# Kernel tuning notes

Hardware: AMD Instinct MI355X
Metric: run time of the kernel (lower is better)

The kernel has to match this reference:

```python
import jax, jax.numpy as jnp
import numpy as np

L, H, DK = 4, 8, 64
NEG = -1e9
PAD = -9999.0


def _ln(z, g, b, eps=1e-6):
    # LayerNormalization: uses unbiased std (torch default) and divides by (std + eps)
    m = jnp.mean(z, axis=-1, keepdims=True)
    s = jnp.std(z, axis=-1, keepdims=True, ddof=1)
    return g * (z - m) / (s + eps) + b


def _mha(q_in, kv_in, w, bw, pw, pb, lnp, mask):
    B, Sq, D = q_in.shape
    q = (q_in @ w[0] + bw[0]).reshape(B, Sq, H, DK).transpose(0, 2, 1, 3)
    k = (kv_in @ w[1] + bw[1]).reshape(B, -1, H, DK).transpose(0, 2, 1, 3)
    v = (kv_in @ w[2] + bw[2]).reshape(B, -1, H, DK).transpose(0, 2, 1, 3)
    scores = jnp.einsum('bhqd,bhkd->bhqk', q, k) * (1.0 / np.sqrt(DK))
    if mask is not None:
        scores = jnp.where(mask[:, None, :, :], NEG, scores)
    attn = jax.nn.softmax(scores, axis=-1)
    ctx = jnp.einsum('bhqk,bhkd->bhqd', attn, v).transpose(0, 2, 1, 3).reshape(B, Sq, H * DK)
    return _ln(q_in + ctx @ pw + pb, lnp[0], lnp[1])


def _ffn(x, w1, b1, w2, b2, lnp):
    # kernel-1 conv1d == pointwise linear; w1:[d_ff,d_model], w2:[d_model,d_ff]
    h = jax.nn.relu(jnp.einsum('bsd,fd->bsf', x, w1) + b1)
    o = jnp.einsum('bsf,df->bsd', h, w2) + b2
    return _ln(x + o, lnp[0], lnp[1])


def _forward(enc_inputs, dec_inputs, emb_w, emb_b, pos_table,
             e_qkv_w, e_qkv_b, e_pw, e_pb, e_ln1, e_w1, e_b1, e_w2, e_b2, e_ln2,
             ds_qkv_w, ds_qkv_b, ds_pw, ds_pb, d_ln1,
             dc_qkv_w, dc_qkv_b, dc_pw, dc_pb, d_ln2,
             d_w1, d_b1, d_w2, d_b2, d_ln3):
    B, Se, F = enc_inputs.shape
    Sd = dec_inputs.shape[1]
    # ConvEmbeddingLayer: kernel-1 conv producing (d_model - n_features) channels, concat with raw inputs
    enc = jnp.concatenate([enc_inputs, jnp.einsum('bsf,of->bso', enc_inputs, emb_w) + emb_b], axis=-1)
    dec = jnp.concatenate([dec_inputs, jnp.einsum('bsf,of->bso', dec_inputs, emb_w) + emb_b], axis=-1)
    # PosEncoding with full lengths -> rows 1..S of the padded table
    enc = enc + pos_table[1:Se + 1]
    dec = dec + pos_table[1:Sd + 1]
    # masks per get_attn_pad_mask / get_attn_subsequent_mask
    enc_pad = jnp.sum(enc_inputs, axis=-1) <= PAD  # [B,Se]
    dec_pad = jnp.sum(dec_inputs, axis=-1) <= PAD  # [B,Sd]
    enc_mask = jnp.broadcast_to(enc_pad[:, None, :], (B, Se, Se))
    causal = jnp.triu(jnp.ones((Sd, Sd), dtype=bool), 1)
    dec_self_mask = jnp.broadcast_to(dec_pad[:, None, :], (B, Sd, Sd)) | causal
    cross_mask = jnp.broadcast_to(enc_pad[:, None, :], (B, Sd, Se))
    for i in range(L):
        enc = _mha(enc, enc, e_qkv_w[i], e_qkv_b[i], e_pw[i], e_pb[i], e_ln1[i], enc_mask)
        enc = _ffn(enc, e_w1[i], e_b1[i], e_w2[i], e_b2[i], e_ln2[i])
    for i in range(L):
        dec = _mha(dec, dec, ds_qkv_w[i], ds_qkv_b[i], ds_pw[i], ds_pb[i], d_ln1[i], dec_self_mask)
        dec = _mha(dec, enc, dc_qkv_w[i], dc_qkv_b[i], dc_pw[i], dc_pb[i], d_ln2[i], cross_mask)
        dec = _ffn(dec, d_w1[i], d_b1[i], d_w2[i], d_b2[i], d_ln3[i])
    return dec


def setup_inputs() -> dict:
    B, Se, Sd, F, Dm, Dff = 8, 512, 512, 32, 512, 2048
    key = jax.random.key(0)
    ks = iter(jax.random.split(key, 32))
    s = 0.02

    def n(shape, sc=s):
        return jax.random.normal(next(ks), shape, jnp.float32) * sc

    # sinusoidal PosEncoding table with leading pad row
    pos = np.arange(Se, dtype=np.float64)[:, None]
    j = np.arange(Dm)[None, :]
    ang = pos / np.power(10000.0, 2.0 * (j // 2) / Dm)
    ang[:, 0::2] = np.sin(ang[:, 0::2])
    ang[:, 1::2] = np.cos(ang[:, 1::2])
    pos_table = jnp.asarray(np.concatenate([np.zeros((1, Dm)), ang]).astype(np.float32))

    ln = jnp.broadcast_to(jnp.stack([jnp.ones(Dm), jnp.zeros(Dm)]), (L, 2, Dm)).astype(jnp.float32) + 0.0
    return {
        'enc_inputs': jax.random.normal(next(ks), (B, Se, F), jnp.float32),
        'dec_inputs': jax.random.normal(next(ks), (B, Sd, F), jnp.float32),
        'emb_w': n((Dm - F, F)), 'emb_b': jnp.zeros(Dm - F, jnp.float32),
        'pos_table': pos_table,
        'e_qkv_w': n((L, 3, Dm, H * DK)), 'e_qkv_b': jnp.zeros((L, 3, H * DK), jnp.float32),
        'e_pw': n((L, H * DK, Dm)), 'e_pb': jnp.zeros((L, Dm), jnp.float32), 'e_ln1': ln,
        'e_w1': n((L, Dff, Dm)), 'e_b1': jnp.zeros((L, Dff), jnp.float32),
        'e_w2': n((L, Dm, Dff)), 'e_b2': jnp.zeros((L, Dm), jnp.float32), 'e_ln2': ln,
        'ds_qkv_w': n((L, 3, Dm, H * DK)), 'ds_qkv_b': jnp.zeros((L, 3, H * DK), jnp.float32),
        'ds_pw': n((L, H * DK, Dm)), 'ds_pb': jnp.zeros((L, Dm), jnp.float32), 'd_ln1': ln,
        'dc_qkv_w': n((L, 3, Dm, H * DK)), 'dc_qkv_b': jnp.zeros((L, 3, H * DK), jnp.float32),
        'dc_pw': n((L, H * DK, Dm)), 'dc_pb': jnp.zeros((L, Dm), jnp.float32), 'd_ln2': ln,
        'd_w1': n((L, Dff, Dm)), 'd_b1': jnp.zeros((L, Dff), jnp.float32),
        'd_w2': n((L, Dm, Dff)), 'd_b2': jnp.zeros((L, Dm), jnp.float32), 'd_ln3': ln,
    }


def reference(enc_inputs, dec_inputs, emb_w, emb_b, pos_table,
              e_qkv_w, e_qkv_b, e_pw, e_pb, e_ln1, e_w1, e_b1, e_w2, e_b2, e_ln2,
              ds_qkv_w, ds_qkv_b, ds_pw, ds_pb, d_ln1,
              dc_qkv_w, dc_qkv_b, dc_pw, dc_pb, d_ln2,
              d_w1, d_b1, d_w2, d_b2, d_ln3):
    return _forward(enc_inputs, dec_inputs, emb_w, emb_b, pos_table,
                    e_qkv_w, e_qkv_b, e_pw, e_pb, e_ln1, e_w1, e_b1, e_w2, e_b2, e_ln2,
                    ds_qkv_w, ds_qkv_b, ds_pw, ds_pb, d_ln1,
                    dc_qkv_w, dc_qkv_b, dc_pw, dc_pb, d_ln2,
                    d_w1, d_b1, d_w2, d_b2, d_ln3)
```

## Files before the change

### kernel.cpp

```cpp
#include <hip/hip_runtime.h>
#include <cstdint>
#include <cstddef>

typedef unsigned short u16;
typedef __bf16 bf16x8 __attribute__((ext_vector_type(8)));
typedef float f32x4 __attribute__((ext_vector_type(4)));

constexpr int Bz = 8, Sq = 512, Hh = 8, DKd = 64, Dm = 512, Dff = 2048, NL = 4;
constexpr int TOK = Bz * Sq;
constexpr size_t MAT = (size_t)512 * 512;
constexpr size_t EL  = (size_t)TOK * Dm;
constexpr size_t WFT = (size_t)Dff * Dm;

__device__ __forceinline__ float bf2f(u16 u) {
  union { uint32_t i; float f; } v; v.i = (uint32_t)u << 16; return v.f;
}
__device__ __forceinline__ u16 f2bf(float f) {
  union { float f; uint32_t i; } v; v.f = f;
  uint32_t i = v.i;
  i += 0x7fffu + ((i >> 16) & 1u);
  return (u16)(i >> 16);
}

__device__ __forceinline__ void gload16(const u16* g, u16* l) {
  __builtin_amdgcn_global_load_lds(
      (const __attribute__((address_space(1))) unsigned int*)g,
      (__attribute__((address_space(3))) unsigned int*)l, 16, 0, 0);
}

template<int BM, int BN>
__global__ __launch_bounds__(256)
void gemm_tile(const u16* __restrict__ A, const u16* __restrict__ Bt,
               const float* __restrict__ bias, u16* __restrict__ C,
               int K, int lda, long long sA, int ldb, long long sB,
               int ldc, long long sC, int cmode, int relu, int colofs,
               const u16* A2, int xsplit, const float* __restrict__ posp)
{
  constexpr int HM = BM / 2, HN = BN / 2, MI = HM / 16, NI = HN / 16;
  __shared__ __align__(16) u16 As[BM * 64];
  __shared__ __align__(16) u16 Bs[BN * 64];
  const int bz = blockIdx.z;
  const u16* Abase = A;
  int colbase;
  if (A2 && (int)blockIdx.x >= xsplit) {
    Abase = A2;
    colbase = 512 + ((int)blockIdx.x - xsplit) * BN;
  } else {
    colbase = colofs + (int)blockIdx.x * BN;
  }
  const u16* Ab = Abase + (size_t)bz * (size_t)sA + (size_t)(blockIdx.y * BM) * lda;
  const u16* Bb = Bt + (size_t)bz * (size_t)sB + (size_t)colbase * ldb;
  const int tid  = threadIdx.x;
  const int lane = tid & 63;
  const int wid  = tid >> 6;
  const int l15  = lane & 15;
  const int quad = lane >> 4;
  const int wm   = wid >> 1, wn = wid & 1;

  f32x4 acc[MI][NI] = {};

  for (int k0 = 0; k0 < K; k0 += 64) {
#pragma unroll
    for (int i = 0; i < BM / 32; ++i) {
      const int s = tid + i * 256;
      const int row = s >> 3, c = (s & 7) ^ (row & 7);
      gload16(Ab + (size_t)row * lda + k0 + c * 8, As + s * 8);
    }
#pragma unroll
    for (int i = 0; i < BN / 32; ++i) {
      const int s = tid + i * 256;
      const int row = s >> 3, c = (s & 7) ^ (row & 7);
      gload16(Bb + (size_t)row * ldb + k0 + c * 8, Bs + s * 8);
    }
    __syncthreads();
#pragma unroll
    for (int kk = 0; kk < 2; ++kk) {
      bf16x8 af[MI], bfr[NI];
#pragma unroll
      for (int mi = 0; mi < MI; ++mi) {
        const int ra = wm * HM + mi * 16 + l15;
        af[mi] = *(const bf16x8*)(As + ra * 64 + (((kk * 4 + quad) ^ (ra & 7))) * 8);
      }
#pragma unroll
      for (int ni = 0; ni < NI; ++ni) {
        const int rb = wn * HN + ni * 16 + l15;
        bfr[ni] = *(const bf16x8*)(Bs + rb * 64 + (((kk * 4 + quad) ^ (rb & 7))) * 8);
      }
#pragma unroll
      for (int mi = 0; mi < MI; ++mi)
#pragma unroll
        for (int ni = 0; ni < NI; ++ni)
          acc[mi][ni] = __builtin_amdgcn_mfma_f32_16x16x32_bf16(af[mi], bfr[ni], acc[mi][ni], 0, 0, 0);
    }
    __syncthreads();
  }

  const int rblk = blockIdx.y * BM + wm * HM + quad * 4;
#pragma unroll
  for (int ni = 0; ni < NI; ++ni) {
    const int colx = colbase + wn * HN + ni * 16 + l15;
    const float bv = bias ? bias[colx] : 0.f;
#pragma unroll
    for (int mi = 0; mi < MI; ++mi) {
#pragma unroll
      for (int r = 0; r < 4; ++r) {
        float v = acc[mi][ni][r] + bv;
        if (relu) v = fmaxf(v, 0.f);
        const int grow = rblk + mi * 16 + r;
        size_t off;
        if (cmode == 0) {
          off = (size_t)bz * (size_t)sC + (size_t)grow * ldc + colx;
        } else if (cmode == 5) {
          const int s = grow & 511;
          v += posp[(size_t)(s + 1) * 512 + colx];
          off = (size_t)grow * 512 + colx;
        } else {
          const int sec = colx >> 9, n = colx & 511, h = n >> 6, d = n & 63;
          const int b = grow >> 9, s = grow & 511;
          if (sec == 0) v *= 0.125f;
          if (sec < 2) off = (size_t)sec * EL + (size_t)b * 262144 + (size_t)h * 32768 + (size_t)s * 64 + d;
          else         off = 2 * EL + (size_t)b * 262144 + (size_t)h * 32768 + (size_t)d * 512 + s;
        }
        C[off] = f2bf(v);
      }
    }
  }
}

__global__ __launch_bounds__(256)
void flash_attn(const u16* __restrict__ q, const u16* __restrict__ k,
                const u16* __restrict__ v, const unsigned char* __restrict__ pad,
                u16* __restrict__ ctx, int mtype)
{
  __shared__ __align__(16) u16 KVs[8192];
  __shared__ __align__(16) u16 Pw[4][2048];
  const int bh = blockIdx.y, b = bh >> 3, h = bh & 7;
  const int qt = blockIdx.x;
  const int tid = threadIdx.x, lane = tid & 63, wid = tid >> 6;
  const int l15 = lane & 15, quad = lane >> 4;
  const size_t bho = (size_t)bh * 32768;
  const int qrow = qt * 64 + wid * 16 + l15;
  const int qcd  = qt * 64 + wid * 16 + quad * 4;

  unsigned char* Ps = (unsigned char*)&Pw[0][0];
  if (tid < 128) ((uchar4*)Ps)[tid] = ((const uchar4*)(pad + b * 512))[tid];

  bf16x8 aq0 = *(const bf16x8*)(q + bho + (size_t)qrow * 64 + quad * 8);
  bf16x8 aq1 = *(const bf16x8*)(q + bho + (size_t)qrow * 64 + 32 + quad * 8);

  f32x4 S[32];
#pragma unroll
  for (int kc = 0; kc < 4; ++kc) {
    __syncthreads();
#pragma unroll
    for (int i = 0; i < 4; ++i) {
      const int s = tid + i * 256;
      const int row = s >> 3, c = (s & 7) ^ (row & 7);
      gload16(k + bho + (size_t)(kc * 128 + row) * 64 + c * 8, KVs + s * 8);
    }
    __syncthreads();
#pragma unroll
    for (int t = 0; t < 8; ++t) {
      const int sw = l15 & 7;
      bf16x8 b0 = *(const bf16x8*)(KVs + (t * 16 + l15) * 64 + (quad ^ sw) * 8);
      bf16x8 b1 = *(const bf16x8*)(KVs + (t * 16 + l15) * 64 + ((4 + quad) ^ sw) * 8);
      f32x4 z = {0.f, 0.f, 0.f, 0.f};
      z = __builtin_amdgcn_mfma_f32_16x16x32_bf16(aq0, b0, z, 0, 0, 0);
      S[kc * 8 + t] = __builtin_amdgcn_mfma_f32_16x16x32_bf16(aq1, b1, z, 0, 0, 0);
    }
  }

  unsigned pm = 0u;
#pragma unroll
  for (int t = 0; t < 32; ++t) pm |= (unsigned)(Ps[t * 16 + l15] != 0) << t;

  float inv[4];
#pragma unroll
  for (int r = 0; r < 4; ++r) {
    const int qg = qcd + r;
    float mx = -3.0e38f;
#pragma unroll
    for (int t = 0; t < 32; ++t) {
      const int col = t * 16 + l15;
      const bool m = ((pm >> t) & 1u) || (mtype == 1 && col > qg);
      const float val = m ? -1e9f : S[t][r];
      S[t][r] = val;
      mx = fmaxf(mx, val);
    }
#pragma unroll
    for (int o = 8; o > 0; o >>= 1) mx = fmaxf(mx, __shfl_xor(mx, o));
    float sm = 0.f;
#pragma unroll
    for (int t = 0; t < 32; ++t) { const float e = __expf(S[t][r] - mx); S[t][r] = e; sm += e; }
#pragma unroll
    for (int o = 8; o > 0; o >>= 1) sm += __shfl_xor(sm, o);
    inv[r] = 1.f / sm;
  }

  f32x4 O[4] = {};
  u16* myP = &Pw[wid][0];
#pragma unroll
  for (int kc = 0; kc < 4; ++kc) {
    __syncthreads();
#pragma unroll
    for (int i = 0; i < 4; ++i) {
      const int s = tid + i * 256;
      const int row = s >> 4, c = (s & 15) ^ (row & 15);
      gload16(v + bho + (size_t)row * 512 + kc * 128 + c * 8, KVs + s * 8);
    }
#pragma unroll
    for (int t = 0; t < 8; ++t)
#pragma unroll
      for (int r = 0; r < 4; ++r) {
        const int rowq = quad * 4 + r;
        const int c = 2 * t + (l15 >> 3);
        myP[rowq * 128 + (c ^ rowq) * 8 + (l15 & 7)] = f2bf(S[kc * 8 + t][r] * inv[r]);
      }
    __syncthreads();
#pragma unroll
    for (int kk = 0; kk < 4; ++kk) {
      bf16x8 ap = *(const bf16x8*)(myP + l15 * 128 + ((kk * 4 + quad) ^ l15) * 8);
#pragma unroll
      for (int ni = 0; ni < 4; ++ni) {
        bf16x8 bv = *(const bf16x8*)(KVs + (ni * 16 + l15) * 128 + ((kk * 4 + quad) ^ l15) * 8);
        O[ni] = __builtin_amdgcn_mfma_f32_16x16x32_bf16(ap, bv, O[ni], 0, 0, 0);
      }
    }
  }

  const int token = b * 512 + qcd;
#pragma unroll
  for (int ni = 0; ni < 4; ++ni)
#pragma unroll
    for (int r = 0; r < 4; ++r)
      ctx[(size_t)(token + r) * 512 + h * 64 + ni * 16 + l15] = f2bf(O[ni][r]);
}

__global__ __launch_bounds__(256)
void prep_weights(const float* __restrict__ s0, const float* __restrict__ s1,
                  const float* __restrict__ s2, const float* __restrict__ s3,
                  const float* __restrict__ s4, const float* __restrict__ s5,
                  u16* __restrict__ outT,
                  const float* __restrict__ c0, const float* __restrict__ c1,
                  const float* __restrict__ c2, const float* __restrict__ c3,
                  u16* __restrict__ outC,
                  const float* __restrict__ ew, const float* __restrict__ eb,
                  u16* __restrict__ ewb, float* __restrict__ biasE,
                  const float* __restrict__ xe, const float* __restrict__ xd,
                  u16* __restrict__ xbf,
                  unsigned char* __restrict__ pe, unsigned char* __restrict__ pd)
{
  __shared__ float tile[32][33];
  const int z = blockIdx.z;
  const int tid = threadIdx.y * 32 + threadIdx.x;
  if (z < 48) {
    const float* src; int zi;
    if      (z < 12) { src = s0; zi = z; }
    else if (z < 24) { src = s1; zi = z - 12; }
    else if (z < 36) { src = s2; zi = z - 24; }
    else if (z < 40) { src = s3; zi = z - 36; }
    else if (z < 44) { src = s4; zi = z - 40; }
    else             { src = s5; zi = z - 44; }
    const float* in = src + (size_t)zi * MAT;
    u16* o = outT + (size_t)z * MAT;
    const int x = blockIdx.x * 32 + threadIdx.x;
    const int y = blockIdx.y * 32 + threadIdx.y;
#pragma unroll
    for (int i = 0; i < 32; i += 8)
      tile[threadIdx.y + i][threadIdx.x] = in[(size_t)(y + i) * 512 + x];
    __syncthreads();
    const int r  = tid >> 3;
    const int cg = (tid & 7) * 4;
    ushort4 w;
    w.x = f2bf(tile[cg + 0][r]);
    w.y = f2bf(tile[cg + 1][r]);
    w.z = f2bf(tile[cg + 2][r]);
    w.w = f2bf(tile[cg + 3][r]);
    *(ushort4*)(o + (size_t)(blockIdx.x * 32 + r) * 512 + blockIdx.y * 32 + cg) = w;
  } else if (z < 112) {
    const int L = (z - 48) * 256 + blockIdx.y * 16 + blockIdx.x;
    const int tens = L >> 12, bx = L & 4095;
    const float* srcs[4] = { c0, c1, c2, c3 };
    const float* src = srcs[tens];
    u16* dst = outC + (size_t)tens * (4 * WFT);
    const int i = (bx * 256 + tid) * 4;
    float4 v = *(const float4*)(src + i);
    ushort4 u = { f2bf(v.x), f2bf(v.y), f2bf(v.z), f2bf(v.w) };
    *(ushort4*)(dst + i) = u;
  } else if (z == 112) {
    const int bxy = blockIdx.y * 16 + blockIdx.x;
    if (tid < 128) {
      const int row = bxy * 2 + (tid >> 6);
      const int c = tid & 63;
      float v;
      if (row < 32) v = (c == row) ? 1.f : 0.f;
      else          v = (c < 32) ? ew[(size_t)(row - 32) * 32 + c] : 0.f;
      ewb[(size_t)row * 64 + c] = f2bf(v);
    }
    if (bxy == 0) {
#pragma unroll
      for (int rep = 0; rep < 2; ++rep) {
        const int i = tid + rep * 256;
        biasE[i] = (i < 32) ? 0.f : eb[i - 32];
      }
    }
  } else {
    const int bxy = blockIdx.y * 16 + blockIdx.x;
    const int lw = tid & 31;
#pragma unroll
    for (int rep = 0; rep < 4; ++rep) {
      const int r = bxy * 32 + rep * 8 + (tid >> 5);
      const float* xsrc = (r < 4096) ? xe : xd;
      const int rr = r & 4095;
      const float v = xsrc[(size_t)rr * 32 + lw];
      float sm = v;
#pragma unroll
      for (int o = 16; o > 0; o >>= 1) sm += __shfl_xor(sm, o);
      if (lw == 0) {
        unsigned char* pv = (r < 4096) ? pe : pd;
        pv[rr] = (sm <= -9999.f) ? 1 : 0;
      }
      u16* orow = xbf + (size_t)r * 64;
      orow[lw] = f2bf(v);
      orow[32 + lw] = 0;
    }
  }
}

__global__ __launch_bounds__(256)
void add_ln(const u16* __restrict__ x, const u16* __restrict__ y,
            const float* __restrict__ g, const float* __restrict__ bb,
            u16* __restrict__ out, float* __restrict__ out32)
{
  const int row  = blockIdx.x * 4 + (threadIdx.x >> 6);
  const int lane = threadIdx.x & 63;
  const int c0 = lane * 8;
  const size_t base = (size_t)row * Dm + c0;

  uint4 xr = *(const uint4*)(x + base);
  uint4 yr = *(const uint4*)(y + base);
  const u16* xh = (const u16*)&xr;
  const u16* yh = (const u16*)&yr;
  float z[8];
  float s = 0.f;
#pragma unroll
  for (int j = 0; j < 8; ++j) { z[j] = bf2f(xh[j]) + bf2f(yh[j]); s += z[j]; }
#pragma unroll
  for (int off = 32; off > 0; off >>= 1) s += __shfl_xor(s, off);
  const float mean = s * (1.f / 512.f);
  float ss = 0.f;
#pragma unroll
  for (int j = 0; j < 8; ++j) { z[j] -= mean; ss += z[j] * z[j]; }
#pragma unroll
  for (int off = 32; off > 0; off >>= 1) ss += __shfl_xor(ss, off);
  const float stdv = sqrtf(ss * (1.f / 511.f));
  const float inv = 1.f / (stdv + 1e-6f);

  float4 g0 = *(const float4*)(g + c0),  g1 = *(const float4*)(g + c0 + 4);
  float4 b0 = *(const float4*)(bb + c0), b1 = *(const float4*)(bb + c0 + 4);
  float gv[8] = { g0.x, g0.y, g0.z, g0.w, g1.x, g1.y, g1.z, g1.w };
  float bv[8] = { b0.x, b0.y, b0.z, b0.w, b1.x, b1.y, b1.z, b1.w };
  float o[8];
#pragma unroll
  for (int j = 0; j < 8; ++j) o[j] = gv[j] * z[j] * inv + bv[j];
  if (out32) {
    float4 w0 = { o[0], o[1], o[2], o[3] };
    float4 w1 = { o[4], o[5], o[6], o[7] };
    *(float4*)(out32 + base) = w0;
    *(float4*)(out32 + base + 4) = w1;
  } else {
    uint4 ow;
    u16* oh = (u16*)&ow;
#pragma unroll
    for (int j = 0; j < 8; ++j) oh[j] = f2bf(o[j]);
    *(uint4*)(out + base) = ow;
  }
}

extern "C" void kernel_launch(void* const* d_in, const int* in_sizes, int n_in,
                              void* d_out, int out_size, void* d_ws, size_t ws_size,
                              hipStream_t stream)
{
  (void)in_sizes; (void)n_in; (void)out_size;
  const float* enc_in   = (const float*)d_in[0];
  const float* dec_in   = (const float*)d_in[1];
  const float* emb_w    = (const float*)d_in[2];
  const float* emb_b    = (const float*)d_in[3];
  const float* pos      = (const float*)d_in[4];
  const float* e_qkv_w  = (const float*)d_in[5];
  const float* e_qkv_b  = (const float*)d_in[6];
  const float* e_pw     = (const float*)d_in[7];
  const float* e_pb     = (const float*)d_in[8];
  const float* e_ln1    = (const float*)d_in[9];
  const float* e_w1     = (const float*)d_in[10];
  const float* e_b1     = (const float*)d_in[11];
  const float* e_w2     = (const float*)d_in[12];
  const float* e_b2     = (const float*)d_in[13];
  const float* e_ln2    = (const float*)d_in[14];
  const float* ds_qkv_w = (const float*)d_in[15];
  const float* ds_qkv_b = (const float*)d_in[16];
  const float* ds_pw    = (const float*)d_in[17];
  const float* ds_pb    = (const float*)d_in[18];
  const float* d_ln1    = (const float*)d_in[19];
  const float* dc_qkv_w = (const float*)d_in[20];
  const float* dc_qkv_b = (const float*)d_in[21];
  const float* dc_pw    = (const float*)d_in[22];
  const float* dc_pb    = (const float*)d_in[23];
  const float* d_ln2    = (const float*)d_in[24];
  const float* d_w1     = (const float*)d_in[25];
  const float* d_b1     = (const float*)d_in[26];
  const float* d_w2     = (const float*)d_in[27];
  const float* d_b2     = (const float*)d_in[28];
  const float* d_ln3    = (const float*)d_in[29];

  u16* ws  = (u16*)d_ws;
  u16* enc = ws;
  u16* dec = ws + EL;
  u16* qb  = ws + 2 * EL;
  u16* kb  = ws + 3 * EL;
  u16* vT  = ws + 4 * EL;
  u16* ctx = ws + 5 * EL;
  u16* t1  = ws + 6 * EL;
  u16* hff = ws + 7 * EL;
  u16* wT  = ws + 15 * EL;
  unsigned char* padE = (unsigned char*)(ws + 21 * EL);
  unsigned char* padD = padE + TOK;
  u16* xbf   = ws + 21 * EL + 8192;
  u16* ewb   = xbf + (size_t)8192 * 64;
  float* biasE = (float*)(ewb + 32768);
  u16* wfAll = ws + 22 * EL;
  if (ws_size < 30 * EL * 2 + 2 * TOK) return;

  prep_weights<<<dim3(16, 16, 114), dim3(32, 8), 0, stream>>>(
      e_qkv_w, ds_qkv_w, dc_qkv_w, e_pw, ds_pw, dc_pw, wT,
      e_w1, e_w2, d_w1, d_w2, wfAll,
      emb_w, emb_b, ewb, biasE,
      enc_in, dec_in, xbf, padE, padD);
  gemm_tile<64, 128><<<dim3(4, 128, 1), 256, 0, stream>>>(
      xbf, ewb, biasE, enc, 64, 64, 0, 64, 0, 512, 0, 5, 0, 0, nullptr, 0, pos);

  auto attention = [&](const u16* qsrc, const u16* kvsrc, const u16* wq3, const float* b3,
                       const u16* pwT, const float* pb, const float* ln,
                       const unsigned char* pad, int mtype, u16* x) {
    if (qsrc == kvsrc) {
      gemm_tile<64, 128><<<dim3(12, 64, 1), 256, 0, stream>>>(
          qsrc, wq3, b3, qb, 512, 512, 0, 512, 0, 0, 0, 4, 0, 0, nullptr, 0, nullptr);
    } else {
      gemm_tile<64, 128><<<dim3(12, 64, 1), 256, 0, stream>>>(
          qsrc, wq3, b3, qb, 512, 512, 0, 512, 0, 0, 0, 4, 0, 0, kvsrc, 4, nullptr);
    }
    flash_attn<<<dim3(8, 64), 256, 0, stream>>>(qb, kb, vT, pad, ctx, mtype);
    gemm_tile<64, 64><<<dim3(8, 64, 1), 256, 0, stream>>>(
        ctx, pwT, pb, t1, 512, 512, 0, 512, 0, 512, 0, 0, 0, 0, nullptr, 0, nullptr);
    add_ln<<<TOK / 4, 256, 0, stream>>>(x, t1, ln, ln + 512, x, nullptr);
  };

  auto ffn = [&](u16* x, const u16* w1b, const float* b1, const u16* w2b,
                 const float* b2, const float* ln, float* o32) {
    gemm_tile<128, 128><<<dim3(16, 32, 1), 256, 0, stream>>>(
        x, w1b, b1, hff, 512, 512, 0, 512, 0, 2048, 0, 0, 1, 0, nullptr, 0, nullptr);
    gemm_tile<64, 64><<<dim3(8, 64, 1), 256, 0, stream>>>(
        hff, w2b, b2, t1, 2048, 2048, 0, 2048, 0, 512, 0, 0, 0, 0, nullptr, 0, nullptr);
    add_ln<<<TOK / 4, 256, 0, stream>>>(x, t1, ln, ln + 512, x, o32);
  };

  for (int i = 0; i < NL; ++i) {
    attention(enc, enc, wT + (size_t)(i * 3) * MAT, e_qkv_b + i * 3 * 512,
              wT + (size_t)(36 + i) * MAT, e_pb + i * 512, e_ln1 + i * 1024, padE, 0, enc);
    ffn(enc, wfAll + (size_t)i * WFT, e_b1 + i * Dff,
        wfAll + 4 * WFT + (size_t)i * WFT, e_b2 + i * Dm, e_ln2 + i * 1024, nullptr);
  }

  for (int i = 0; i < NL; ++i) {
    attention(dec, dec, wT + (size_t)(12 + i * 3) * MAT, ds_qkv_b + i * 3 * 512,
              wT + (size_t)(40 + i) * MAT, ds_pb + i * 512, d_ln1 + i * 1024, padD, 1, dec);
    attention(dec, enc, wT + (size_t)(24 + i * 3) * MAT, dc_qkv_b + i * 3 * 512,
              wT + (size_t)(44 + i) * MAT, dc_pb + i * 512, d_ln2 + i * 1024, padE, 2, dec);
    ffn(dec, wfAll + 8 * WFT + (size_t)i * WFT, d_b1 + i * Dff,
        wfAll + 12 * WFT + (size_t)i * WFT, d_b2 + i * Dm, d_ln3 + i * 1024,
        (i == NL - 1) ? (float*)d_out : nullptr);
  }
}
```

Baseline: 1.282 ms.

## Double-buffer GEMM LDS tiles to overlap global loads with MFMA compute

```diff
diff --git a/kernel.cpp b/kernel.cpp
--- a/kernel.cpp
+++ b/kernel.cpp
@@ -28,7 +28,7 @@
       (__attribute__((address_space(3))) unsigned int*)l, 16, 0, 0);
 }
 
-template<int BM, int BN>
+template<int BM, int BN, int TAG>
 __global__ __launch_bounds__(256)
 void gemm_tile(const u16* __restrict__ A, const u16* __restrict__ Bt,
                const float* __restrict__ bias, u16* __restrict__ C,
@@ -37,8 +37,10 @@
                const u16* A2, int xsplit, const float* __restrict__ posp)
 {
   constexpr int HM = BM / 2, HN = BN / 2, MI = HM / 16, NI = HN / 16;
-  __shared__ __align__(16) u16 As[BM * 64];
-  __shared__ __align__(16) u16 Bs[BN * 64];
+  constexpr int LV = BM / 32 + BN / 32;
+  static_assert(LV == 4 || LV == 6 || LV == 8, "unsupported tile");
+  __shared__ __align__(16) u16 As[2][BM * 64];
+  __shared__ __align__(16) u16 Bs[2][BN * 64];
   const int bz = blockIdx.z;
   const u16* Abase = A;
   int colbase;
@@ -52,39 +54,41 @@
   const u16* Bb = Bt + (size_t)bz * (size_t)sB + (size_t)colbase * ldb;
   const int tid  = threadIdx.x;
   const int lane = tid & 63;
-  const int wid  = tid >> 6;
   const int l15  = lane & 15;
   const int quad = lane >> 4;
+  const int wid  = tid >> 6;
   const int wm   = wid >> 1, wn = wid & 1;
 
   f32x4 acc[MI][NI] = {};
 
-  for (int k0 = 0; k0 < K; k0 += 64) {
+  auto STAGE = [&](int buf, int k0) {
 #pragma unroll
     for (int i = 0; i < BM / 32; ++i) {
       const int s = tid + i * 256;
       const int row = s >> 3, c = (s & 7) ^ (row & 7);
-      gload16(Ab + (size_t)row * lda + k0 + c * 8, As + s * 8);
+      gload16(Ab + (size_t)row * lda + k0 + c * 8, &As[buf][s * 8]);
     }
 #pragma unroll
     for (int i = 0; i < BN / 32; ++i) {
       const int s = tid + i * 256;
       const int row = s >> 3, c = (s & 7) ^ (row & 7);
-      gload16(Bb + (size_t)row * ldb + k0 + c * 8, Bs + s * 8);
-    }
-    __syncthreads();
+      gload16(Bb + (size_t)row * ldb + k0 + c * 8, &Bs[buf][s * 8]);
+    }
+  };
+
+  auto COMPUTE = [&](int buf) {
 #pragma unroll
     for (int kk = 0; kk < 2; ++kk) {
       bf16x8 af[MI], bfr[NI];
 #pragma unroll
       for (int mi = 0; mi < MI; ++mi) {
         const int ra = wm * HM + mi * 16 + l15;
-        af[mi] = *(const bf16x8*)(As + ra * 64 + (((kk * 4 + quad) ^ (ra & 7))) * 8);
+        af[mi] = *(const bf16x8*)(&As[buf][ra * 64 + (((kk * 4 + quad) ^ (ra & 7))) * 8]);
       }
 #pragma unroll
       for (int ni = 0; ni < NI; ++ni) {
         const int rb = wn * HN + ni * 16 + l15;
-        bfr[ni] = *(const bf16x8*)(Bs + rb * 64 + (((kk * 4 + quad) ^ (rb & 7))) * 8);
+        bfr[ni] = *(const bf16x8*)(&Bs[buf][rb * 64 + (((kk * 4 + quad) ^ (rb & 7))) * 8]);
       }
 #pragma unroll
       for (int mi = 0; mi < MI; ++mi)
@@ -92,8 +96,25 @@
         for (int ni = 0; ni < NI; ++ni)
           acc[mi][ni] = __builtin_amdgcn_mfma_f32_16x16x32_bf16(af[mi], bfr[ni], acc[mi][ni], 0, 0, 0);
     }
-    __syncthreads();
-  }
+  };
+
+  STAGE(0, 0);
+  const int NT = K >> 6;
+  int cur = 0;
+  for (int t = 0; t < NT - 1; ++t) {
+    STAGE(cur ^ 1, (t + 1) << 6);
+    if constexpr (LV == 4)      asm volatile("s_waitcnt vmcnt(4)" ::: "memory");
+    else if constexpr (LV == 6) asm volatile("s_waitcnt vmcnt(6)" ::: "memory");
+    else                        asm volatile("s_waitcnt vmcnt(8)" ::: "memory");
+    __builtin_amdgcn_s_barrier();
+    COMPUTE(cur);
+    asm volatile("s_waitcnt lgkmcnt(0)" ::: "memory");
+    __builtin_amdgcn_s_barrier();
+    cur ^= 1;
+  }
+  asm volatile("s_waitcnt vmcnt(0)" ::: "memory");
+  __builtin_amdgcn_s_barrier();
+  COMPUTE(cur);
 
   const int rblk = blockIdx.y * BM + wm * HM + quad * 4;
 #pragma unroll
@@ -253,6 +274,8 @@
   __shared__ float tile[32][33];
   const int z = blockIdx.z;
   const int tid = threadIdx.y * 32 + threadIdx.x;
+  const int r  = tid >> 3;
+  const int c4 = (tid & 7) * 4;
   if (z < 48) {
     const float* src; int zi;
     if      (z < 12) { src = s0; zi = z; }
@@ -263,20 +286,16 @@
     else             { src = s5; zi = z - 44; }
     const float* in = src + (size_t)zi * MAT;
     u16* o = outT + (size_t)z * MAT;
-    const int x = blockIdx.x * 32 + threadIdx.x;
-    const int y = blockIdx.y * 32 + threadIdx.y;
-#pragma unroll
-    for (int i = 0; i < 32; i += 8)
-      tile[threadIdx.y + i][threadIdx.x] = in[(size_t)(y + i) * 512 + x];
+    float4 v = *(const float4*)(in + (size_t)(blockIdx.y * 32 + r) * 512 + blockIdx.x * 32 + c4);
+    tile[r][c4 + 0] = v.x; tile[r][c4 + 1] = v.y;
+    tile[r][c4 + 2] = v.z; tile[r][c4 + 3] = v.w;
     __syncthreads();
-    const int r  = tid >> 3;
-    const int cg = (tid & 7) * 4;
     ushort4 w;
-    w.x = f2bf(tile[cg + 0][r]);
-    w.y = f2bf(tile[cg + 1][r]);
-    w.z = f2bf(tile[cg + 2][r]);
-    w.w = f2bf(tile[cg + 3][r]);
-    *(ushort4*)(o + (size_t)(blockIdx.x * 32 + r) * 512 + blockIdx.y * 32 + cg) = w;
+    w.x = f2bf(tile[c4 + 0][r]);
+    w.y = f2bf(tile[c4 + 1][r]);
+    w.z = f2bf(tile[c4 + 2][r]);
+    w.w = f2bf(tile[c4 + 3][r]);
+    *(ushort4*)(o + (size_t)(blockIdx.x * 32 + r) * 512 + blockIdx.y * 32 + c4) = w;
   } else if (z < 112) {
     const int L = (z - 48) * 256 + blockIdx.y * 16 + blockIdx.x;
     const int tens = L >> 12, bx = L & 4095;
@@ -309,18 +328,18 @@
     const int lw = tid & 31;
 #pragma unroll
     for (int rep = 0; rep < 4; ++rep) {
-      const int r = bxy * 32 + rep * 8 + (tid >> 5);
-      const float* xsrc = (r < 4096) ? xe : xd;
-      const int rr = r & 4095;
+      const int rr0 = bxy * 32 + rep * 8 + (tid >> 5);
+      const float* xsrc = (rr0 < 4096) ? xe : xd;
+      const int rr = rr0 & 4095;
       const float v = xsrc[(size_t)rr * 32 + lw];
       float sm = v;
 #pragma unroll
       for (int o = 16; o > 0; o >>= 1) sm += __shfl_xor(sm, o);
       if (lw == 0) {
-        unsigned char* pv = (r < 4096) ? pe : pd;
+        unsigned char* pv = (rr0 < 4096) ? pe : pd;
         pv[rr] = (sm <= -9999.f) ? 1 : 0;
       }
-      u16* orow = xbf + (size_t)r * 64;
+      u16* orow = xbf + (size_t)rr0 * 64;
       orow[lw] = f2bf(v);
       orow[32 + lw] = 0;
     }
@@ -436,30 +455,30 @@
       e_w1, e_w2, d_w1, d_w2, wfAll,
       emb_w, emb_b, ewb, biasE,
       enc_in, dec_in, xbf, padE, padD);
-  gemm_tile<64, 128><<<dim3(4, 128, 1), 256, 0, stream>>>(
+  gemm_tile<64, 128, 4><<<dim3(4, 128, 1), 256, 0, stream>>>(
       xbf, ewb, biasE, enc, 64, 64, 0, 64, 0, 512, 0, 5, 0, 0, nullptr, 0, pos);
 
   auto attention = [&](const u16* qsrc, const u16* kvsrc, const u16* wq3, const float* b3,
                        const u16* pwT, const float* pb, const float* ln,
                        const unsigned char* pad, int mtype, u16* x) {
     if (qsrc == kvsrc) {
-      gemm_tile<64, 128><<<dim3(12, 64, 1), 256, 0, stream>>>(
+      gemm_tile<64, 128, 0><<<dim3(12, 64, 1), 256, 0, stream>>>(
           qsrc, wq3, b3, qb, 512, 512, 0, 512, 0, 0, 0, 4, 0, 0, nullptr, 0, nullptr);
     } else {
-      gemm_tile<64, 128><<<dim3(12, 64, 1), 256, 0, stream>>>(
+      gemm_tile<64, 128, 0><<<dim3(12, 64, 1), 256, 0, stream>>>(
           qsrc, wq3, b3, qb, 512, 512, 0, 512, 0, 0, 0, 4, 0, 0, kvsrc, 4, nullptr);
     }
     flash_attn<<<dim3(8, 64), 256, 0, stream>>>(qb, kb, vT, pad, ctx, mtype);
-    gemm_tile<64, 64><<<dim3(8, 64, 1), 256, 0, stream>>>(
+    gemm_tile<64, 64, 1><<<dim3(8, 64, 1), 256, 0, stream>>>(
         ctx, pwT, pb, t1, 512, 512, 0, 512, 0, 512, 0, 0, 0, 0, nullptr, 0, nullptr);
     add_ln<<<TOK / 4, 256, 0, stream>>>(x, t1, ln, ln + 512, x, nullptr);
   };
 
   auto ffn = [&](u16* x, const u16* w1b, const float* b1, const u16* w2b,
                  const float* b2, const float* ln, float* o32) {
-    gemm_tile<128, 128><<<dim3(16, 32, 1), 256, 0, stream>>>(
+    gemm_tile<64, 128, 2><<<dim3(16, 64, 1), 256, 0, stream>>>(
         x, w1b, b1, hff, 512, 512, 0, 512, 0, 2048, 0, 0, 1, 0, nullptr, 0, nullptr);
-    gemm_tile<64, 64><<<dim3(8, 64, 1), 256, 0, stream>>>(
+    gemm_tile<64, 64, 3><<<dim3(8, 64, 1), 256, 0, stream>>>(
         hff, w2b, b2, t1, 2048, 2048, 0, 2048, 0, 512, 0, 0, 0, 0, nullptr, 0, nullptr);
     add_ln<<<TOK / 4, 256, 0, stream>>>(x, t1, ln, ln + 512, x, o32);
   };
```

New measurement: 1.294 ms. Within noise of the previous version (+0.9%).

## Fuse output-projection and FFN2 GEMMs with residual add and LayerNorm

Applied to the files above, without the earlier changes.

```diff
diff --git a/kernel.cpp b/kernel.cpp
--- a/kernel.cpp
+++ b/kernel.cpp
@@ -28,7 +28,7 @@
       (__attribute__((address_space(3))) unsigned int*)l, 16, 0, 0);
 }
 
-template<int BM, int BN>
+template<int BM, int BN, int TAG>
 __global__ __launch_bounds__(256)
 void gemm_tile(const u16* __restrict__ A, const u16* __restrict__ Bt,
                const float* __restrict__ bias, u16* __restrict__ C,
@@ -127,6 +127,124 @@
   }
 }
 
+template<int K, int TAG>
+__global__ __launch_bounds__(256)
+void gemm_row_ln(const u16* __restrict__ A, const u16* __restrict__ Bt,
+                 const float* __restrict__ bias, const u16* __restrict__ resid,
+                 const float* __restrict__ g, const float* __restrict__ bb,
+                 u16* __restrict__ out, float* __restrict__ out32)
+{
+  __shared__ __align__(16) u16 Bs[512 * 64];
+  __shared__ __align__(16) u16 As[16 * 64];
+  __shared__ float redS[4][16], redQ[4][16];
+  const int tid = threadIdx.x, lane = tid & 63, wid = tid >> 6;
+  const int l15 = lane & 15, quad = lane >> 4;
+  const int r0 = blockIdx.x * 16;
+  const u16* Ab = A + (size_t)r0 * K;
+
+  f32x4 acc[8] = {};
+  for (int k0 = 0; k0 < K; k0 += 64) {
+    if (tid < 128) {
+      const int row = tid >> 3, c = (tid & 7) ^ (row & 7);
+      gload16(Ab + (size_t)row * K + k0 + c * 8, As + tid * 8);
+    }
+#pragma unroll
+    for (int i = 0; i < 16; ++i) {
+      const int s = tid + i * 256;
+      const int row = s >> 3, c = (s & 7) ^ (row & 7);
+      gload16(Bt + (size_t)row * K + k0 + c * 8, Bs + s * 8);
+    }
+    __syncthreads();
+#pragma unroll
+    for (int kk = 0; kk < 2; ++kk) {
+      bf16x8 af = *(const bf16x8*)(As + l15 * 64 + (((kk * 4 + quad) ^ (l15 & 7))) * 8);
+#pragma unroll
+      for (int ni = 0; ni < 8; ++ni) {
+        const int rb = wid * 128 + ni * 16 + l15;
+        bf16x8 bf = *(const bf16x8*)(Bs + rb * 64 + (((kk * 4 + quad) ^ (rb & 7))) * 8);
+        acc[ni] = __builtin_amdgcn_mfma_f32_16x16x32_bf16(af, bf, acc[ni], 0, 0, 0);
+      }
+    }
+    __syncthreads();
+  }
+
+  float z[8][4];
+  float s[4] = {0.f, 0.f, 0.f, 0.f}, q[4] = {0.f, 0.f, 0.f, 0.f};
+#pragma unroll
+  for (int ni = 0; ni < 8; ++ni) {
+    const int colx = wid * 128 + ni * 16 + l15;
+    const float bv = bias[colx];
+#pragma unroll
+    for (int r = 0; r < 4; ++r) {
+      const int row = quad * 4 + r;
+      const float zz = acc[ni][r] + bv + bf2f(resid[(size_t)(r0 + row) * 512 + colx]);
+      z[ni][r] = zz; s[r] += zz; q[r] += zz * zz;
+    }
+  }
+#pragma unroll
+  for (int r = 0; r < 4; ++r) {
+#pragma unroll
+    for (int m = 8; m > 0; m >>= 1) {
+      s[r] += __shfl_xor(s[r], m);
+      q[r] += __shfl_xor(q[r], m);
+    }
+  }
+  if (l15 == 0) {
+#pragma unroll
+    for (int r = 0; r < 4; ++r) {
+      redS[wid][quad * 4 + r] = s[r];
+      redQ[wid][quad * 4 + r] = q[r];
+    }
+  }
+  __syncthreads();
+  float mean[4], inv[4];
+#pragma unroll
+  for (int r = 0; r < 4; ++r) {
+    const int row = quad * 4 + r;
+    const float sT = redS[0][row] + redS[1][row] + redS[2][row] + redS[3][row];
+    const float qT = redQ[0][row] + redQ[1][row] + redQ[2][row] + redQ[3][row];
+    mean[r] = sT * (1.f / 512.f);
+    const float ssc = fmaxf(qT - 512.f * mean[r] * mean[r], 0.f);
+    const float stdv = sqrtf(ssc * (1.f / 511.f));
+    inv[r] = 1.f / (stdv + 1e-6f);
+  }
+  __syncthreads();
+  u16* Ls = Bs;
+#pragma unroll
+  for (int ni = 0; ni < 8; ++ni) {
+    const int colx = wid * 128 + ni * 16 + l15;
+    const float gv = g[colx], bvv = bb[colx];
+#pragma unroll
+    for (int r = 0; r < 4; ++r) {
+      const int row = quad * 4 + r;
+      Ls[row * 512 + colx] = f2bf(gv * (z[ni][r] - mean[r]) * inv[r] + bvv);
+    }
+  }
+  __syncthreads();
+  if (out32) {
+#pragma unroll
+    for (int i = 0; i < 4; ++i) {
+      const int idx = tid + i * 256;
+      const int row = idx >> 6, c8 = idx & 63;
+      uint4 raw = *(const uint4*)(Ls + (size_t)row * 512 + c8 * 8);
+      const u16* h = (const u16*)&raw;
+      float4 o0 = { bf2f(h[0]), bf2f(h[1]), bf2f(h[2]), bf2f(h[3]) };
+      float4 o1 = { bf2f(h[4]), bf2f(h[5]), bf2f(h[6]), bf2f(h[7]) };
+      float* dst = out32 + (size_t)(r0 + row) * 512 + c8 * 8;
+      *(float4*)dst = o0;
+      *(float4*)(dst + 4) = o1;
+    }
+  } else {
+#pragma unroll
+    for (int i = 0; i < 4; ++i) {
+      const int idx = tid + i * 256;
+      const int row = idx >> 6, c8 = idx & 63;
+      *(uint4*)(out + (size_t)(r0 + row) * 512 + c8 * 8) =
+          *(const uint4*)(Ls + (size_t)row * 512 + c8 * 8);
+    }
+  }
+}
+
 __global__ __launch_bounds__(256)
 void flash_attn(const u16* __restrict__ q, const u16* __restrict__ k,
                 const u16* __restrict__ v, const unsigned char* __restrict__ pad,
@@ -250,10 +368,12 @@
                   u16* __restrict__ xbf,
                   unsigned char* __restrict__ pe, unsigned char* __restrict__ pd)
 {
-  __shared__ float tile[32][33];
-  const int z = blockIdx.z;
-  const int tid = threadIdx.y * 32 + threadIdx.x;
-  if (z < 48) {
+  __shared__ float tile[64][65];
+  const int blk = blockIdx.x;
+  const int tid = threadIdx.x;
+  if (blk < 3072) {
+    const int z = blk >> 6, t = blk & 63;
+    const int tx = t & 7, ty = t >> 3;
     const float* src; int zi;
     if      (z < 12) { src = s0; zi = z; }
     else if (z < 24) { src = s1; zi = z - 12; }
@@ -263,117 +383,75 @@
     else             { src = s5; zi = z - 44; }
     const float* in = src + (size_t)zi * MAT;
     u16* o = outT + (size_t)z * MAT;
-    const int x = blockIdx.x * 32 + threadIdx.x;
-    const int y = blockIdx.y * 32 + threadIdx.y;
-#pragma unroll
-    for (int i = 0; i < 32; i += 8)
-      tile[threadIdx.y + i][threadIdx.x] = in[(size_t)(y + i) * 512 + x];
-    __syncthreads();
-    const int r  = tid >> 3;
-    const int cg = (tid & 7) * 4;
-    ushort4 w;
-    w.x = f2bf(tile[cg + 0][r]);
-    w.y = f2bf(tile[cg + 1][r]);
-    w.z = f2bf(tile[cg + 2][r]);
-    w.w = f2bf(tile[cg + 3][r]);
-    *(ushort4*)(o + (size_t)(blockIdx.x * 32 + r) * 512 + blockIdx.y * 32 + cg) = w;
-  } else if (z < 112) {
-    const int L = (z - 48) * 256 + blockIdx.y * 16 + blockIdx.x;
-    const int tens = L >> 12, bx = L & 4095;
+    const int rr = tid >> 4, slot = tid & 15;
+#pragma unroll
+    for (int j = 0; j < 4; ++j) {
+      const int row = j * 16 + rr;
+      float4 v = *(const float4*)(in + (size_t)(ty * 64 + row) * 512 + tx * 64 + slot * 4);
+      tile[row][slot * 4 + 0] = v.x; tile[row][slot * 4 + 1] = v.y;
+      tile[row][slot * 4 + 2] = v.z; tile[row][slot * 4 + 3] = v.w;
+    }
+    __syncthreads();
+#pragma unroll
+    for (int j = 0; j < 4; ++j) {
+      const int row = j * 16 + rr;
+      ushort4 w;
+      w.x = f2bf(tile[slot * 4 + 0][row]);
+      w.y = f2bf(tile[slot * 4 + 1][row]);
+      w.z = f2bf(tile[slot * 4 + 2][row]);
+      w.w = f2bf(tile[slot * 4 + 3][row]);
+      *(ushort4*)(o + (size_t)(tx * 64 + row) * 512 + ty * 64 + slot * 4) = w;
+    }
+  } else if (blk < 7168) {
+    const int L = blk - 3072;
+    const size_t e0 = (size_t)L * 4096 + (size_t)tid * 16;
+    const int tens = (int)(e0 >> 22);
+    const size_t local = e0 & (4 * WFT - 1);
     const float* srcs[4] = { c0, c1, c2, c3 };
     const float* src = srcs[tens];
-    u16* dst = outC + (size_t)tens * (4 * WFT);
-    const int i = (bx * 256 + tid) * 4;
-    float4 v = *(const float4*)(src + i);
-    ushort4 u = { f2bf(v.x), f2bf(v.y), f2bf(v.z), f2bf(v.w) };
-    *(ushort4*)(dst + i) = u;
-  } else if (z == 112) {
-    const int bxy = blockIdx.y * 16 + blockIdx.x;
-    if (tid < 128) {
-      const int row = bxy * 2 + (tid >> 6);
-      const int c = tid & 63;
+    u16* dst = outC + (size_t)tens * (4 * WFT) + local;
+#pragma unroll
+    for (int j = 0; j < 4; ++j) {
+      float4 v = *(const float4*)(src + local + j * 4);
+      ushort4 u = { f2bf(v.x), f2bf(v.y), f2bf(v.z), f2bf(v.w) };
+      *(ushort4*)(dst + j * 4) = u;
+    }
+  } else if (blk < 7184) {
+    const int j = blk - 7168;
+    const int row = j * 32 + (tid >> 3);
+    const int c0i = (tid & 7) * 8;
+#pragma unroll
+    for (int k = 0; k < 8; ++k) {
+      const int c = c0i + k;
       float v;
       if (row < 32) v = (c == row) ? 1.f : 0.f;
       else          v = (c < 32) ? ew[(size_t)(row - 32) * 32 + c] : 0.f;
       ewb[(size_t)row * 64 + c] = f2bf(v);
     }
-    if (bxy == 0) {
-#pragma unroll
-      for (int rep = 0; rep < 2; ++rep) {
-        const int i = tid + rep * 256;
-        biasE[i] = (i < 32) ? 0.f : eb[i - 32];
-      }
+    if (j == 0) {
+      biasE[tid]       = (tid < 32) ? 0.f : eb[tid - 32];
+      biasE[tid + 256] = eb[tid + 256 - 32];
     }
   } else {
-    const int bxy = blockIdx.y * 16 + blockIdx.x;
+    const int bxy = blk - 7184;
     const int lw = tid & 31;
 #pragma unroll
     for (int rep = 0; rep < 4; ++rep) {
-      const int r = bxy * 32 + rep * 8 + (tid >> 5);
-      const float* xsrc = (r < 4096) ? xe : xd;
-      const int rr = r & 4095;
+      const int rr0 = bxy * 32 + rep * 8 + (tid >> 5);
+      const float* xsrc = (rr0 < 4096) ? xe : xd;
+      const int rr = rr0 & 4095;
       const float v = xsrc[(size_t)rr * 32 + lw];
       float sm = v;
 #pragma unroll
       for (int o = 16; o > 0; o >>= 1) sm += __shfl_xor(sm, o);
       if (lw == 0) {
-        unsigned char* pv = (r < 4096) ? pe : pd;
+        unsigned char* pv = (rr0 < 4096) ? pe : pd;
         pv[rr] = (sm <= -9999.f) ? 1 : 0;
       }
-      u16* orow = xbf + (size_t)r * 64;
+      u16* orow = xbf + (size_t)rr0 * 64;
       orow[lw] = f2bf(v);
       orow[32 + lw] = 0;
     }
-  }
-}
-
-__global__ __launch_bounds__(256)
-void add_ln(const u16* __restrict__ x, const u16* __restrict__ y,
-            const float* __restrict__ g, const float* __restrict__ bb,
-            u16* __restrict__ out, float* __restrict__ out32)
-{
-  const int row  = blockIdx.x * 4 + (threadIdx.x >> 6);
-  const int lane = threadIdx.x & 63;
-  const int c0 = lane * 8;
-  const size_t base = (size_t)row * Dm + c0;
-
-  uint4 xr = *(const uint4*)(x + base);
-  uint4 yr = *(const uint4*)(y + base);
-  const u16* xh = (const u16*)&xr;
-  const u16* yh = (const u16*)&yr;
-  float z[8];
-  float s = 0.f;
-#pragma unroll
-  for (int j = 0; j < 8; ++j) { z[j] = bf2f(xh[j]) + bf2f(yh[j]); s += z[j]; }
-#pragma unroll
-  for (int off = 32; off > 0; off >>= 1) s += __shfl_xor(s, off);
-  const float mean = s * (1.f / 512.f);
-  float ss = 0.f;
-#pragma unroll
-  for (int j = 0; j < 8; ++j) { z[j] -= mean; ss += z[j] * z[j]; }
-#pragma unroll
-  for (int off = 32; off > 0; off >>= 1) ss += __shfl_xor(ss, off);
-  const float stdv = sqrtf(ss * (1.f / 511.f));
-  const float inv = 1.f / (stdv + 1e-6f);
-
-  float4 g0 = *(const float4*)(g + c0),  g1 = *(const float4*)(g + c0 + 4);
-  float4 b0 = *(const float4*)(bb + c0), b1 = *(const float4*)(bb + c0 + 4);
-  float gv[8] = { g0.x, g0.y, g0.z, g0.w, g1.x, g1.y, g1.z, g1.w };
-  float bv[8] = { b0.x, b0.y, b0.z, b0.w, b1.x, b1.y, b1.z, b1.w };
-  float o[8];
-#pragma unroll
-  for (int j = 0; j < 8; ++j) o[j] = gv[j] * z[j] * inv + bv[j];
-  if (out32) {
-    float4 w0 = { o[0], o[1], o[2], o[3] };
-    float4 w1 = { o[4], o[5], o[6], o[7] };
-    *(float4*)(out32 + base) = w0;
-    *(float4*)(out32 + base + 4) = w1;
-  } else {
-    uint4 ow;
-    u16* oh = (u16*)&ow;
-#pragma unroll
-    for (int j = 0; j < 8; ++j) oh[j] = f2bf(o[j]);
-    *(uint4*)(out + base) = ow;
   }
 }
 
@@ -420,7 +498,6 @@
   u16* kb  = ws + 3 * EL;
   u16* vT  = ws + 4 * EL;
   u16* ctx = ws + 5 * EL;
-  u16* t1  = ws + 6 * EL;
   u16* hff = ws + 7 * EL;
   u16* wT  = ws + 15 * EL;
   unsigned char* padE = (unsigned char*)(ws + 21 * EL);
@@ -431,37 +508,35 @@
   u16* wfAll = ws + 22 * EL;
   if (ws_size < 30 * EL * 2 + 2 * TOK) return;
 
-  prep_weights<<<dim3(16, 16, 114), dim3(32, 8), 0, stream>>>(
+  prep_weights<<<7440, 256, 0, stream>>>(
       e_qkv_w, ds_qkv_w, dc_qkv_w, e_pw, ds_pw, dc_pw, wT,
       e_w1, e_w2, d_w1, d_w2, wfAll,
       emb_w, emb_b, ewb, biasE,
       enc_in, dec_in, xbf, padE, padD);
-  gemm_tile<64, 128><<<dim3(4, 128, 1), 256, 0, stream>>>(
+  gemm_tile<64, 128, 4><<<dim3(4, 128, 1), 256, 0, stream>>>(
       xbf, ewb, biasE, enc, 64, 64, 0, 64, 0, 512, 0, 5, 0, 0, nullptr, 0, pos);
 
   auto attention = [&](const u16* qsrc, const u16* kvsrc, const u16* wq3, const float* b3,
                        const u16* pwT, const float* pb, const float* ln,
                        const unsigned char* pad, int mtype, u16* x) {
     if (qsrc == kvsrc) {
-      gemm_tile<64, 128><<<dim3(12, 64, 1), 256, 0, stream>>>(
+      gemm_tile<64, 128, 0><<<dim3(12, 64, 1), 256, 0, stream>>>(
           qsrc, wq3, b3, qb, 512, 512, 0, 512, 0, 0, 0, 4, 0, 0, nullptr, 0, nullptr);
     } else {
-      gemm_tile<64, 128><<<dim3(12, 64, 1), 256, 0, stream>>>(
+      gemm_tile<64, 128, 0><<<dim3(12, 64, 1), 256, 0, stream>>>(
           qsrc, wq3, b3, qb, 512, 512, 0, 512, 0, 0, 0, 4, 0, 0, kvsrc, 4, nullptr);
     }
     flash_attn<<<dim3(8, 64), 256, 0, stream>>>(qb, kb, vT, pad, ctx, mtype);
-    gemm_tile<64, 64><<<dim3(8, 64, 1), 256, 0, stream>>>(
-        ctx, pwT, pb, t1, 512, 512, 0, 512, 0, 512, 0, 0, 0, 0, nullptr, 0, nullptr);
-    add_ln<<<TOK / 4, 256, 0, stream>>>(x, t1, ln, ln + 512, x, nullptr);
+    gemm_row_ln<512, 0><<<256, 256, 0, stream>>>(
+        ctx, pwT, pb, x, ln, ln + 512, x, nullptr);
   };
 
   auto ffn = [&](u16* x, const u16* w1b, const float* b1, const u16* w2b,
                  const float* b2, const float* ln, float* o32) {
-    gemm_tile<128, 128><<<dim3(16, 32, 1), 256, 0, stream>>>(
+    gemm_tile<64, 128, 2><<<dim3(16, 64, 1), 256, 0, stream>>>(
         x, w1b, b1, hff, 512, 512, 0, 512, 0, 2048, 0, 0, 1, 0, nullptr, 0, nullptr);
-    gemm_tile<64, 64><<<dim3(8, 64, 1), 256, 0, stream>>>(
-        hff, w2b, b2, t1, 2048, 2048, 0, 2048, 0, 512, 0, 0, 0, 0, nullptr, 0, nullptr);
-    add_ln<<<TOK / 4, 256, 0, stream>>>(x, t1, ln, ln + 512, x, o32);
+    gemm_row_ln<2048, 1><<<256, 256, 0, stream>>>(
+        hff, w2b, b2, x, ln, ln + 512, x, o32);
   };
 
   for (int i = 0; i < NL; ++i) {
```

Measured after the change: 1.395 ms. +8.8%, slower.
